# Performance work log

Hardware: AMD Instinct MI355X
Metric: run time of the kernel (lower is better)

## Reference

```python
import jax, jax.numpy as jnp
import numpy as np

# --- SLAYER params (nmnistNet.yaml) ---
THETA = 10.0
TS = 1.0
TAU_REF = 1.0
SCALE_REF = 2.0
T_SAMPLE = 300
B = 8

def _alpha_kernel(tau, mult, t_sample, ts, eps=0.01):
    vals = []
    t = 0.0
    while t < t_sample:
        v = mult * t / tau * np.exp(1.0 - t / tau)
        if abs(v) < eps and t > tau:
            break
        vals.append(v)
        t += ts
    return np.asarray(vals, np.float32)

# refractory kernel: alpha kernel with mult = -scaleRef*theta (slayer._calculateRefKernel)
REF_KERNEL = _alpha_kernel(TAU_REF, -SCALE_REF * THETA, T_SAMPLE, TS)
NREF = REF_KERNEL.shape[0]  # 11 for these params; REF_KERNEL[0] == 0


def spike(u):
    """slayerCuda.getSpikes: per-neuron sequential threshold recurrence over time.
    u: [..., T] membrane potential. On spike at t, REF_KERNEL is accumulated
    into u[t:t+NREF]; spike amplitude is 1/Ts."""
    uT = jnp.moveaxis(u, -1, 0)  # [T, ...]
    refk = jnp.asarray(REF_KERNEL[1:]).reshape((NREF - 1,) + (1,) * (u.ndim - 1))
    buf0 = jnp.zeros((NREF - 1,) + uT.shape[1:], u.dtype)  # pending refractory

    def step(buf, u_t):
        u_mod = u_t + buf[0]
        ev = (u_mod >= THETA).astype(u.dtype)
        buf = jnp.concatenate([buf[1:], jnp.zeros_like(buf[:1])], axis=0) + ev[None] * refk
        return buf, ev / TS

    _, s = jax.lax.scan(step, buf0, uT)
    return jnp.moveaxis(s, 0, -1)


def conv2d_t(x, w, pad):
    """slayer.conv: Conv3d with kernel (k,k,1) == per-timestep 2D conv.
    x: [B,C,H,W,T], w: [O,I,kh,kw]."""
    b, c, h, wd, t = x.shape
    xb = jnp.moveaxis(x, -1, 1).reshape(b * t, c, h, wd)
    y = jax.lax.conv_general_dilated(xb, w, (1, 1), [(pad, pad), (pad, pad)],
                                     dimension_numbers=('NCHW', 'OIHW', 'NCHW'))
    o, ho, wo = y.shape[1], y.shape[2], y.shape[3]
    return jnp.moveaxis(y.reshape(b, t, o, ho, wo), 1, -1)


def sum_pool2(x):
    """slayer.pool(2): fixed-weight (1.1*theta) 2x2/stride-2 sum over H,W per channel."""
    y = jax.lax.reduce_window(x, 0.0, jax.lax.add, (1, 1, 2, 2, 1), (1, 1, 2, 2, 1), 'VALID')
    return 1.1 * THETA * y


def setup_inputs():
    key = jax.random.key(0)
    k0, k1, k2, k3, k4 = jax.random.split(key, 5)
    spikeInput = (jax.random.uniform(k0, (B, 2, 34, 34, T_SAMPLE)) < 0.1).astype(jnp.float32) / TS
    # conv weights: kaiming-uniform bound * 100 (the __init__ scales conv weights by 100)
    w1 = jax.random.uniform(k1, (16, 2, 5, 5), minval=-14.1, maxval=14.1, dtype=jnp.float32)
    w2 = jax.random.uniform(k2, (32, 16, 3, 3), minval=-8.3, maxval=8.3, dtype=jnp.float32)
    w3 = jax.random.uniform(k3, (64, 32, 3, 3), minval=-5.9, maxval=5.9, dtype=jnp.float32)
    wfc = jax.random.uniform(k4, (10, 64, 8, 8), minval=-0.5, maxval=0.5, dtype=jnp.float32)
    return {"spikeInput": spikeInput, "w1": w1, "w2": w2, "w3": w3, "wfc": wfc}


def reference(spikeInput, w1, w2, w3, wfc):
    s1 = spike(conv2d_t(spikeInput, w1, 1))  # [B,16,32,32,T]
    s2 = spike(sum_pool2(s1))                # [B,16,16,16,T]
    s3 = spike(conv2d_t(s2, w2, 1))          # [B,32,16,16,T]
    s4 = spike(sum_pool2(s3))                # [B,32,8,8,T]
    s5 = spike(conv2d_t(s4, w3, 1))          # [B,64,8,8,T]
    # dense((8,8,64),10): Conv3d(64,10,(8,8,1)) == full-spatial contraction
    u = jnp.einsum('bchwt,ochw->bot', s5, wfc)[:, :, None, None, :]
    return spike(u)                          # [B,10,1,1,T]
```

## Files before the change

### kernel.cpp

```cpp
#include <hip/hip_runtime.h>
#include <hip/hip_bf16.h>
#include <cmath>

#define T_SAMPLE 300
#define NCHUNK 75

typedef __attribute__((ext_vector_type(8))) short short8;
typedef __attribute__((ext_vector_type(4))) float f32x4;

struct RefK { float v[10]; };

__device__ __forceinline__ unsigned char spike_step(float u, float* buf, const RefK& rk) {
    const float um = u + buf[0];
    const bool fire = um >= 10.0f;
    const float ev = fire ? 1.0f : 0.0f;
#pragma unroll
    for (int r = 0; r < 9; ++r) buf[r] = fmaf(ev, rk.v[r], buf[r + 1]);
    buf[9] = ev * rk.v[9];
    return fire ? (unsigned char)1 : (unsigned char)0;
}

__device__ __forceinline__ short8 bytes_to_bf16x8(uint2 w8) {
    union { uint4 u; short8 s8; } cv;
    cv.u.x = (w8.x & 0xFFu) * 0x3F80u | ((((w8.x >> 8) & 0xFFu) * 0x3F80u) << 16);
    cv.u.y = ((w8.x >> 16) & 0xFFu) * 0x3F80u | ((((w8.x >> 24) & 0xFFu) * 0x3F80u) << 16);
    cv.u.z = (w8.y & 0xFFu) * 0x3F80u | ((((w8.y >> 8) & 0xFFu) * 0x3F80u) << 16);
    cv.u.w = ((w8.y >> 16) & 0xFFu) * 0x3F80u | ((((w8.y >> 24) & 0xFFu) * 0x3F80u) << 16);
    return cv.s8;
}

__global__ __launch_bounds__(256) void transpose_in_k(
    const float* __restrict__ In, unsigned int* __restrict__ X)
{
    __shared__ unsigned int lds[16 * NCHUNK];
    const int blk = blockIdx.x;
    const int tn = threadIdx.x >> 4;
    const int tq = threadIdx.x & 15;
    const size_t n = (size_t)blk * 16 + tn;
#pragma unroll
    for (int p = 0; p < 5; ++p) {
        const int ch = p * 16 + tq;
        if (ch < NCHUNK) {
            const float4 v = *(const float4*)(In + n * T_SAMPLE + ch * 4);
            unsigned int u = (v.x != 0.f ? 1u : 0u) | (v.y != 0.f ? 0x100u : 0u) |
                             (v.z != 0.f ? 0x10000u : 0u) | (v.w != 0.f ? 0x1000000u : 0u);
            lds[tn * NCHUNK + ch] = u;
        }
    }
    __syncthreads();
    for (int idx = threadIdx.x; idx < 16 * NCHUNK; idx += 256) {
        const int ch = idx >> 4, t2 = idx & 15;
        X[(size_t)ch * 18496 + blk * 16 + t2] = lds[t2 * NCHUNK + ch];
    }
}

template <int IC, int OC, int K, int OH, int OW, int IH, int IW, int OPT, int CSPLIT>
__device__ __forceinline__ void conv_body(
    const uchar4* __restrict__ in_, const float* __restrict__ W,
    float4* __restrict__ U, int b0, int nbl)
{
    constexpr int TH = 8, TW = 8;
    constexpr int EH = TH + K - 1, EW = TW + K - 1;
    constexpr int EWP = EW + 1;
    constexpr int NTX = OW / TW, NTY = OH / TH, NT = NTX * NTY;
    constexpr int KK = K * K;
    constexpr int ICH = IC / CSPLIT;
    constexpr int ES = ICH * EH * EW;
    constexpr int PLANE_IN = 8 * IC * IH * IW;
    const int PLANE_U = nbl * OC * OH * OW;

    __shared__ float4 tile[ICH * EH * EWP];

    const int tc = blockIdx.x;
    const int by = blockIdx.y;
    const int til = by % NT;
    const int og = by / NT;
    const int ty = til / NTX, tx = til % NTX;
    const int bl = blockIdx.z;
    const int b = b0 + bl;
    const int tid = threadIdx.x;
    const int wave = tid >> 6, lane = tid & 63;
    const int py = lane >> 3, px = lane & 7;

    const int iy0 = ty * TH - 1, ix0 = tx * TW - 1;
    const uchar4* ib = in_ + (size_t)tc * PLANE_IN + (size_t)b * IC * IH * IW;

    float acc[OPT][4];
#pragma unroll
    for (int j = 0; j < OPT; ++j)
#pragma unroll
        for (int k = 0; k < 4; ++k) acc[j][k] = 0.f;

    int ob = (og * 4 + wave) * OPT;
    ob = __builtin_amdgcn_readfirstlane(ob);
    const float* Wp = W + (size_t)ob * IC * KK;

    for (int s = 0; s < CSPLIT; ++s) {
        if (s > 0) __syncthreads();
        for (int e = tid; e < ES; e += 256) {
            const int cl = e / (EH * EW);
            const int r = e % (EH * EW);
            const int iy = r / EW, ix = r % EW;
            const int gy = iy0 + iy, gx = ix0 + ix;
            float4 v = make_float4(0.f, 0.f, 0.f, 0.f);
            if ((unsigned)gy < (unsigned)IH && (unsigned)gx < (unsigned)IW) {
                const uchar4 sv = ib[((s * ICH + cl) * IH + gy) * IW + gx];
                v = make_float4((float)sv.x, (float)sv.y, (float)sv.z, (float)sv.w);
            }
            tile[(cl * EH + iy) * EWP + ix] = v;
        }
        __syncthreads();

        for (int cl = 0; cl < ICH; ++cl) {
            const int c = s * ICH + cl;
#pragma unroll
            for (int dy = 0; dy < K; ++dy) {
                float wr[OPT][K];
#pragma unroll
                for (int j = 0; j < OPT; ++j)
#pragma unroll
                    for (int dx = 0; dx < K; ++dx)
                        wr[j][dx] = Wp[(j * IC + c) * KK + dy * K + dx];
#pragma unroll
                for (int dx = 0; dx < K; ++dx) {
                    const float4 v = tile[((cl * EH) + py + dy) * EWP + (px + dx)];
#pragma unroll
                    for (int j = 0; j < OPT; ++j) {
                        const float w = wr[j][dx];
                        acc[j][0] = fmaf(w, v.x, acc[j][0]);
                        acc[j][1] = fmaf(w, v.y, acc[j][1]);
                        acc[j][2] = fmaf(w, v.z, acc[j][2]);
                        acc[j][3] = fmaf(w, v.w, acc[j][3]);
                    }
                }
            }
        }
    }

    const int y = ty * TH + py, x = tx * TW + px;
#pragma unroll
    for (int j = 0; j < OPT; ++j) {
        const int nb = ((bl * OC + (ob + j)) * OH + y) * OW + x;
        U[(size_t)tc * PLANE_U + nb] = make_float4(acc[j][0], acc[j][1], acc[j][2], acc[j][3]);
    }
}

__global__ __launch_bounds__(256) void conv1_k(
    const uchar4* __restrict__ in_, const float* __restrict__ W,
    float4* __restrict__ U, int b0, int nbl)
{ conv_body<2, 16, 5, 32, 32, 34, 34, 4, 1>(in_, W, U, b0, nbl); }

__global__ __launch_bounds__(256) void prep_w3_k(
    const float* __restrict__ w3, unsigned short* __restrict__ Wr)
{
    const int g = blockIdx.x * 256 + threadIdx.x;
    const int j = g & 7;
    const int lane = (g >> 3) & 63;
    const int mt = (g >> 9) & 3;
    const int rest = g >> 11;
    const int ks = rest % 9;
    const int s = rest / 9;
    const int oc = mt * 16 + (lane & 15);
    const int ic = (lane >> 4) * 8 + j;
    const float w = w3[(oc * 32 + ic) * 9 + ks];
    __hip_bfloat16 hb = __float2bfloat16(w);
    const float hf = __bfloat162float(hb);
    __hip_bfloat16 mb = __float2bfloat16(w - hf);
    const float mf = __bfloat162float(mb);
    __hip_bfloat16 lb = __float2bfloat16(w - hf - mf);
    __hip_bfloat16 sel = (s == 0) ? hb : ((s == 1) ? mb : lb);
    Wr[g] = *(unsigned short*)&sel;
}

__global__ __launch_bounds__(256) void prep_w2_k(
    const float* __restrict__ w2, unsigned short* __restrict__ Wr2)
{
    const int g = blockIdx.x * 256 + threadIdx.x;
    const int j = g & 7;
    const int lane = (g >> 3) & 63;
    const int mt = (g >> 9) & 1;
    const int rest = g >> 10;
    const int kp = rest % 5;
    const int s = rest / 5;
    const int q = lane >> 4;
    const int oc = mt * 16 + (lane & 15);
    const int tap = kp * 2 + (q >> 1);
    const int ic = (q & 1) * 8 + j;
    const float w = (tap <= 8) ? w2[(oc * 16 + ic) * 9 + tap] : 0.f;
    __hip_bfloat16 hb = __float2bfloat16(w);
    const float hf = __bfloat162float(hb);
    __hip_bfloat16 mb = __float2bfloat16(w - hf);
    const float mf = __bfloat162float(mb);
    __hip_bfloat16 lb = __float2bfloat16(w - hf - mf);
    __hip_bfloat16 sel = (s == 0) ? hb : ((s == 1) ? mb : lb);
    Wr2[g] = *(unsigned short*)&sel;
}

__global__ __launch_bounds__(256) void conv2_mfma_k(
    const unsigned int* __restrict__ s2u, const unsigned short* __restrict__ Wr2,
    float4* __restrict__ U, int b0, int nbl)
{
    __shared__ __align__(16) unsigned char pad[4 * 18 * 18 * 16];
    const int tc = blockIdx.x;
    const int bl = blockIdx.z;
    const int b = b0 + bl;
    const int tid = threadIdx.x;
    const int wv = tid >> 6, lane = tid & 63;
    const int q = lane >> 4, n = lane & 15;
    const int PLANE_U = nbl * 8192;

    unsigned int* lp = (unsigned int*)pad;
    for (int i = tid; i < 5184; i += 256) lp[i] = 0u;
    __syncthreads();
    const unsigned int* sb = s2u + (size_t)tc * 32768 + b * 4096;
    for (int e = tid; e < 4096; e += 256) {
        const unsigned int v = sb[e];
        const int c = e >> 8, pix = e & 255;
        const int base = (((pix >> 4) + 1) * 18 + ((pix & 15) + 1)) * 16 + c;
        pad[base]         = (unsigned char)(v & 0xFFu);
        pad[5184 + base]  = (unsigned char)((v >> 8) & 0xFFu);
        pad[10368 + base] = (unsigned char)((v >> 16) & 0xFFu);
        pad[15552 + base] = (unsigned char)(v >> 24);
    }
    __syncthreads();

    for (int i = 0; i < 4; ++i) {
        const int r = wv * 4 + i;
        f32x4 acc[2][4];
#pragma unroll
        for (int mt = 0; mt < 2; ++mt)
#pragma unroll
            for (int t = 0; t < 4; ++t) acc[mt][t] = (f32x4){0.f, 0.f, 0.f, 0.f};

        for (int kp = 0; kp < 5; ++kp) {
            short8 Af[6];
#pragma unroll
            for (int s = 0; s < 3; ++s)
#pragma unroll
                for (int mt = 0; mt < 2; ++mt)
                    Af[s * 2 + mt] = *(const short8*)(Wr2 + ((((s * 5 + kp) * 2 + mt) * 64 + lane) * 8));
            int tap = kp * 2 + (q >> 1);
            if (tap > 8) tap = 8;
            const int dy = tap / 3, dx = tap % 3;
#pragma unroll
            for (int t = 0; t < 4; ++t) {
                const int off = ((t * 18 + r + dy) * 18 + (n + dx)) * 16 + (q & 1) * 8;
                const short8 Bf = bytes_to_bf16x8(*(const uint2*)(pad + off));
#pragma unroll
                for (int s = 0; s < 3; ++s)
#pragma unroll
                    for (int mt = 0; mt < 2; ++mt)
                        acc[mt][t] = __builtin_amdgcn_mfma_f32_16x16x32_bf16(
                            Af[s * 2 + mt], Bf, acc[mt][t], 0, 0, 0);
            }
        }

        const size_t ub = (size_t)tc * PLANE_U;
#pragma unroll
        for (int mt = 0; mt < 2; ++mt)
#pragma unroll
            for (int rr = 0; rr < 4; ++rr) {
                const int oc = mt * 16 + q * 4 + rr;
                const int nb = (bl * 32 + oc) * 256 + r * 16 + n;
                U[ub + nb] = make_float4(acc[mt][0][rr], acc[mt][1][rr], acc[mt][2][rr], acc[mt][3][rr]);
            }
    }
}

__global__ __launch_bounds__(256) void conv3_mfma_k(
    const unsigned int* __restrict__ s4u, const unsigned short* __restrict__ Wr,
    float4* __restrict__ U)
{
    __shared__ __align__(16) unsigned char pad[12800];
    const int tc = blockIdx.x;
    const int bl = blockIdx.z;
    const int tid = threadIdx.x;
    const int wv = tid >> 6, lane = tid & 63;
    const int q = lane >> 4, n = lane & 15;

    unsigned int* lp = (unsigned int*)pad;
    for (int i = tid; i < 3200; i += 256) lp[i] = 0u;
    __syncthreads();
    const unsigned int* sb = s4u + (size_t)tc * 16384 + bl * 2048;
    for (int e = tid; e < 2048; e += 256) {
        const unsigned int v = sb[e];
        const int c = e >> 6, pix = e & 63;
        const int base = (((pix >> 3) + 1) * 10 + ((pix & 7) + 1)) * 32 + c;
        pad[base]        = (unsigned char)(v & 0xFFu);
        pad[3200 + base] = (unsigned char)((v >> 8) & 0xFFu);
        pad[6400 + base] = (unsigned char)((v >> 16) & 0xFFu);
        pad[9600 + base] = (unsigned char)(v >> 24);
    }
    __syncthreads();

    const int pixel = wv * 16 + n;
    const int py0 = pixel >> 3, px0 = pixel & 7;

    f32x4 acc[4][4];
#pragma unroll
    for (int mt = 0; mt < 4; ++mt)
#pragma unroll
        for (int t = 0; t < 4; ++t) acc[mt][t] = (f32x4){0.f, 0.f, 0.f, 0.f};

    for (int ks = 0; ks < 9; ++ks) {
        const int dy = ks / 3, dx = ks % 3;
        short8 Af[12];
#pragma unroll
        for (int s = 0; s < 3; ++s)
#pragma unroll
            for (int mt = 0; mt < 4; ++mt)
                Af[s * 4 + mt] = *(const short8*)(Wr + ((((s * 9 + ks) * 4 + mt) * 64 + lane) * 8));
#pragma unroll
        for (int t = 0; t < 4; ++t) {
            const int off = ((t * 10 + py0 + dy) * 10 + (px0 + dx)) * 32 + q * 8;
            const short8 Bf = bytes_to_bf16x8(*(const uint2*)(pad + off));
#pragma unroll
            for (int s = 0; s < 3; ++s)
#pragma unroll
                for (int mt = 0; mt < 4; ++mt)
                    acc[mt][t] = __builtin_amdgcn_mfma_f32_16x16x32_bf16(
                        Af[s * 4 + mt], Bf, acc[mt][t], 0, 0, 0);
        }
    }

    const size_t ub = (size_t)tc * 32768 + (size_t)bl * 4096;
#pragma unroll
    for (int mt = 0; mt < 4; ++mt)
#pragma unroll
        for (int r = 0; r < 4; ++r) {
            const int oc = mt * 16 + q * 4 + r;
            const int nb = oc * 64 + wv * 16 + n;
            U[ub + nb] = make_float4(acc[mt][0][r], acc[mt][1][r], acc[mt][2][r], acc[mt][3][r]);
        }
}

__device__ __forceinline__ void spike_body(
    const float4* __restrict__ U, uchar4* __restrict__ S,
    int nneur, int sstride, int soff, const RefK& rk)
{
    const int n = blockIdx.x * 64 + threadIdx.x;
    const float4* up = U + n;
    uchar4* sp = S + soff + n;
    float buf[10];
#pragma unroll
    for (int r = 0; r < 10; ++r) buf[r] = 0.f;

    float4 ring[8];
#pragma unroll
    for (int r = 0; r < 8; ++r) ring[r] = up[(size_t)r * nneur];

#pragma unroll 8
    for (int ch = 0; ch < 72; ++ch) {
        const float4 cur = ring[ch & 7];
        const int pf = (ch + 8 < NCHUNK) ? ch + 8 : NCHUNK - 1;
        ring[ch & 7] = up[(size_t)pf * nneur];
        uchar4 o;
        o.x = spike_step(cur.x, buf, rk);
        o.y = spike_step(cur.y, buf, rk);
        o.z = spike_step(cur.z, buf, rk);
        o.w = spike_step(cur.w, buf, rk);
        sp[(size_t)ch * sstride] = o;
    }
#pragma unroll
    for (int ch = 72; ch < NCHUNK; ++ch) {
        const float4 cur = ring[ch & 7];
        uchar4 o;
        o.x = spike_step(cur.x, buf, rk);
        o.y = spike_step(cur.y, buf, rk);
        o.z = spike_step(cur.z, buf, rk);
        o.w = spike_step(cur.w, buf, rk);
        sp[(size_t)ch * sstride] = o;
    }
}

__global__ __launch_bounds__(64) void spike1_k(
    const float4* U, uchar4* S, int nneur, int sstride, int soff, RefK rk)
{ spike_body(U, S, nneur, sstride, soff, rk); }

__global__ __launch_bounds__(64) void spike2_k(
    const float4* U, uchar4* S, int nneur, int sstride, int soff, RefK rk)
{ spike_body(U, S, nneur, sstride, soff, rk); }

__global__ __launch_bounds__(64) void spike3_k(
    const float4* U, uchar4* S, int nneur, int sstride, int soff, RefK rk)
{ spike_body(U, S, nneur, sstride, soff, rk); }

__device__ __forceinline__ int bsum4(uint2 r0, uint2 r1, int k) {
    return (int)((r0.x >> (8 * k)) & 0xffu) + (int)((r0.y >> (8 * k)) & 0xffu)
         + (int)((r1.x >> (8 * k)) & 0xffu) + (int)((r1.y >> (8 * k)) & 0xffu);
}

template <int C, int H, int W>
__device__ __forceinline__ void pool_body(
    const uchar4* __restrict__ Sin, uchar4* __restrict__ Sout, const RefK& rk)
{
    constexpr int H2 = H / 2, W2 = W / 2;
    constexpr int SIN = 8 * C * H * W;
    constexpr int SOUT = 8 * C * H2 * W2;
    const int n = blockIdx.x * 64 + threadIdx.x;
    const int x = n % W2;
    const int y = (n / W2) % H2;
    const int c = (n / (W2 * H2)) % C;
    const int b = n / (W2 * H2 * C);
    const int base = (((b * C + c) * H + 2 * y) * W + 2 * x);
    uchar4* q = Sout + n;

    float buf[10];
#pragma unroll
    for (int r = 0; r < 10; ++r) buf[r] = 0.f;

    uint2 r0[8], r1[8];
#pragma unroll
    for (int r = 0; r < 8; ++r) {
        r0[r] = *(const uint2*)(Sin + (size_t)r * SIN + base);
        r1[r] = *(const uint2*)(Sin + (size_t)r * SIN + base + W);
    }

#pragma unroll 8
    for (int ch = 0; ch < 72; ++ch) {
        const uint2 a0 = r0[ch & 7], a1 = r1[ch & 7];
        const int pf = (ch + 8 < NCHUNK) ? ch + 8 : NCHUNK - 1;
        r0[ch & 7] = *(const uint2*)(Sin + (size_t)pf * SIN + base);
        r1[ch & 7] = *(const uint2*)(Sin + (size_t)pf * SIN + base + W);
        uchar4 o;
        o.x = spike_step(11.0f * (float)bsum4(a0, a1, 0), buf, rk);
        o.y = spike_step(11.0f * (float)bsum4(a0, a1, 1), buf, rk);
        o.z = spike_step(11.0f * (float)bsum4(a0, a1, 2), buf, rk);
        o.w = spike_step(11.0f * (float)bsum4(a0, a1, 3), buf, rk);
        q[(size_t)ch * SOUT] = o;
    }
#pragma unroll
    for (int ch = 72; ch < NCHUNK; ++ch) {
        const uint2 a0 = r0[ch & 7], a1 = r1[ch & 7];
        uchar4 o;
        o.x = spike_step(11.0f * (float)bsum4(a0, a1, 0), buf, rk);
        o.y = spike_step(11.0f * (float)bsum4(a0, a1, 1), buf, rk);
        o.z = spike_step(11.0f * (float)bsum4(a0, a1, 2), buf, rk);
        o.w = spike_step(11.0f * (float)bsum4(a0, a1, 3), buf, rk);
        q[(size_t)ch * SOUT] = o;
    }
}

__global__ __launch_bounds__(64) void pool2_k(
    const uchar4* Sin, uchar4* Sout, RefK rk) { pool_body<16, 32, 32>(Sin, Sout, rk); }
__global__ __launch_bounds__(64) void pool4_k(
    const uchar4* Sin, uchar4* Sout, RefK rk) { pool_body<32, 16, 16>(Sin, Sout, rk); }

__global__ __launch_bounds__(64) void dense_k(
    const uchar4* __restrict__ S5, const float* __restrict__ WFC,
    float4* __restrict__ U6)
{
    const int tc = blockIdx.x, o = blockIdx.y, b = blockIdx.z;
    const int lane = threadIdx.x;
    float a0 = 0.f, a1 = 0.f, a2 = 0.f, a3 = 0.f;
    const uchar4* sb = S5 + (size_t)tc * 32768 + b * 4096;
    const float* wb = WFC + o * 4096;
    for (int i = 0; i < 64; ++i) {
        const int site = i * 64 + lane;
        const uchar4 s = sb[site];
        const float w = wb[site];
        a0 = fmaf(w, (float)s.x, a0);
        a1 = fmaf(w, (float)s.y, a1);
        a2 = fmaf(w, (float)s.z, a2);
        a3 = fmaf(w, (float)s.w, a3);
    }
#pragma unroll
    for (int m = 1; m < 64; m <<= 1) {
        a0 += __shfl_xor(a0, m, 64);
        a1 += __shfl_xor(a1, m, 64);
        a2 += __shfl_xor(a2, m, 64);
        a3 += __shfl_xor(a3, m, 64);
    }
    if (lane == 0)
        U6[(size_t)tc * 80 + b * 10 + o] = make_float4(a0, a1, a2, a3);
}

__global__ __launch_bounds__(128) void spike6_k(
    const float4* __restrict__ U6, float* __restrict__ Out, RefK rk)
{
    const int n = threadIdx.x;
    if (n >= 80) return;
    const float4* up = U6 + n;
    float* op = Out + (size_t)n * T_SAMPLE;
    float buf[10];
#pragma unroll
    for (int r = 0; r < 10; ++r) buf[r] = 0.f;

    float4 ring[8];
#pragma unroll
    for (int r = 0; r < 8; ++r) ring[r] = up[(size_t)r * 80];

#pragma unroll 8
    for (int ch = 0; ch < 72; ++ch) {
        const float4 cur = ring[ch & 7];
        const int pf = (ch + 8 < NCHUNK) ? ch + 8 : NCHUNK - 1;
        ring[ch & 7] = up[(size_t)pf * 80];
        float4 o;
        o.x = (float)spike_step(cur.x, buf, rk);
        o.y = (float)spike_step(cur.y, buf, rk);
        o.z = (float)spike_step(cur.z, buf, rk);
        o.w = (float)spike_step(cur.w, buf, rk);
        *(float4*)(op + ch * 4) = o;
    }
#pragma unroll
    for (int ch = 72; ch < NCHUNK; ++ch) {
        const float4 cur = ring[ch & 7];
        float4 o;
        o.x = (float)spike_step(cur.x, buf, rk);
        o.y = (float)spike_step(cur.y, buf, rk);
        o.z = (float)spike_step(cur.z, buf, rk);
        o.w = (float)spike_step(cur.w, buf, rk);
        *(float4*)(op + ch * 4) = o;
    }
}

extern "C" void kernel_launch(void* const* d_in, const int* in_sizes, int n_in,
                              void* d_out, int out_size, void* d_ws, size_t ws_size,
                              hipStream_t stream)
{
    const float* spikeIn = (const float*)d_in[0];
    const float* w1 = (const float*)d_in[1];
    const float* w2 = (const float*)d_in[2];
    const float* w3 = (const float*)d_in[3];
    const float* wfc = (const float*)d_in[4];
    float* out = (float*)d_out;

    RefK rk;
    for (int t = 1; t <= 10; ++t)
        rk.v[t - 1] = (float)(-20.0 * (double)t * std::exp(1.0 - (double)t));

    const size_t A_BYTES = 39321600;
    const size_t B_BYTES = 9830400;
    const size_t U6_BYTES = 96000;
    const size_t U_HUGE = 157286400, U_BIG = 78643200, U_SMALL = 39321600;
    const size_t TAIL = A_BYTES + B_BYTES + U6_BYTES;
    const bool huge = ws_size >= U_HUGE + TAIL;
    const bool big = ws_size >= U_BIG + TAIL;
    const size_t U_BYTES = huge ? U_HUGE : (big ? U_BIG : U_SMALL);

    char* ws = (char*)d_ws;
    float4* U = (float4*)ws;
    uchar4* A = (uchar4*)(ws + U_BYTES);
    uchar4* Bb = (uchar4*)(ws + U_BYTES + A_BYTES);
    float4* U6 = (float4*)(ws + U_BYTES + A_BYTES + B_BYTES);
    unsigned short* Wr = (unsigned short*)(ws + U_BYTES + 20971520);
    unsigned short* Wr2 = (unsigned short*)(ws + U_BYTES + 20971520 + 131072);

    uchar4* X = Bb;
    uchar4* s1 = A;
    uchar4* s2 = Bb;
    uchar4* s3 = A;
    uchar4* s4 = Bb;
    uchar4* s5 = A;

    transpose_in_k<<<18496 / 16, 256, 0, stream>>>(spikeIn, (unsigned int*)X);

    const int nbl1 = huge ? 8 : (big ? 4 : 2);
    for (int b0 = 0; b0 < 8; b0 += nbl1) {
        dim3 g1(NCHUNK, 16, nbl1);
        conv1_k<<<g1, 256, 0, stream>>>(X, w1, U, b0, nbl1);
        const int nn = nbl1 * 16384;
        spike1_k<<<nn / 64, 64, 0, stream>>>(U, s1, nn, 131072, b0 * 16384, rk);
    }
    pool2_k<<<32768 / 64, 64, 0, stream>>>(s1, s2, rk);
    prep_w2_k<<<60, 256, 0, stream>>>(w2, Wr2);
    prep_w3_k<<<216, 256, 0, stream>>>(w3, Wr);
    const int nbl2 = (huge || big) ? 8 : 4;
    for (int b0 = 0; b0 < 8; b0 += nbl2) {
        dim3 g2(NCHUNK, 1, nbl2);
        conv2_mfma_k<<<g2, 256, 0, stream>>>((const unsigned int*)s2, Wr2, U, b0, nbl2);
        const int nn = nbl2 * 8192;
        spike2_k<<<nn / 64, 64, 0, stream>>>(U, s3, nn, 65536, b0 * 8192, rk);
    }
    pool4_k<<<16384 / 64, 64, 0, stream>>>(s3, s4, rk);
    {
        dim3 g3(NCHUNK, 1, 8);
        conv3_mfma_k<<<g3, 256, 0, stream>>>((const unsigned int*)s4, Wr, U);
        spike3_k<<<32768 / 64, 64, 0, stream>>>(U, s5, 32768, 32768, 0, rk);
    }
    dim3 g6(NCHUNK, 10, 8);
    dense_k<<<g6, 64, 0, stream>>>(s5, wfc, U6);
    spike6_k<<<1, 128, 0, stream>>>(U6, out, rk);
}
```

Before: 300.9 us.

## Port conv1 to bf16 MFMA with split-weight precision and packed spike tiles

Replaces the scalar FP32 conv1 kernel with an MFMA-based version. The weights are pre-split into three bf16 parts (hi/mid/lo) so the FP32 result is kept nearly exact. The binary spike inputs are packed into LDS as bytes and expanded to bf16 fragments, and the 5x5x2 taps are laid out into a 6-wide slot K dimension. This is meant to cut conv1's FP32 FMA cost by using matrix cores. In exchange it adds a weight-prep kernel, does three MFMA passes per tap group, and carries some zero-padded slots.

```diff
diff --git a/kernel.cpp b/kernel.cpp
--- a/kernel.cpp
+++ b/kernel.cpp
@@ -29,6 +29,16 @@
     return cv.s8;
 }
 
+__device__ __forceinline__ unsigned short bf16_split_sel(float w, int s) {
+    __hip_bfloat16 hb = __float2bfloat16(w);
+    const float hf = __bfloat162float(hb);
+    __hip_bfloat16 mb = __float2bfloat16(w - hf);
+    const float mf = __bfloat162float(mb);
+    __hip_bfloat16 lb = __float2bfloat16(w - hf - mf);
+    __hip_bfloat16 sel = (s == 0) ? hb : ((s == 1) ? mb : lb);
+    return *(unsigned short*)&sel;
+}
+
 __global__ __launch_bounds__(256) void transpose_in_k(
     const float* __restrict__ In, unsigned int* __restrict__ X)
 {
@@ -54,101 +64,22 @@
     }
 }
 
-template <int IC, int OC, int K, int OH, int OW, int IH, int IW, int OPT, int CSPLIT>
-__device__ __forceinline__ void conv_body(
-    const uchar4* __restrict__ in_, const float* __restrict__ W,
-    float4* __restrict__ U, int b0, int nbl)
-{
-    constexpr int TH = 8, TW = 8;
-    constexpr int EH = TH + K - 1, EW = TW + K - 1;
-    constexpr int EWP = EW + 1;
-    constexpr int NTX = OW / TW, NTY = OH / TH, NT = NTX * NTY;
-    constexpr int KK = K * K;
-    constexpr int ICH = IC / CSPLIT;
-    constexpr int ES = ICH * EH * EW;
-    constexpr int PLANE_IN = 8 * IC * IH * IW;
-    const int PLANE_U = nbl * OC * OH * OW;
-
-    __shared__ float4 tile[ICH * EH * EWP];
-
-    const int tc = blockIdx.x;
-    const int by = blockIdx.y;
-    const int til = by % NT;
-    const int og = by / NT;
-    const int ty = til / NTX, tx = til % NTX;
-    const int bl = blockIdx.z;
-    const int b = b0 + bl;
-    const int tid = threadIdx.x;
-    const int wave = tid >> 6, lane = tid & 63;
-    const int py = lane >> 3, px = lane & 7;
-
-    const int iy0 = ty * TH - 1, ix0 = tx * TW - 1;
-    const uchar4* ib = in_ + (size_t)tc * PLANE_IN + (size_t)b * IC * IH * IW;
-
-    float acc[OPT][4];
-#pragma unroll
-    for (int j = 0; j < OPT; ++j)
-#pragma unroll
-        for (int k = 0; k < 4; ++k) acc[j][k] = 0.f;
-
-    int ob = (og * 4 + wave) * OPT;
-    ob = __builtin_amdgcn_readfirstlane(ob);
-    const float* Wp = W + (size_t)ob * IC * KK;
-
-    for (int s = 0; s < CSPLIT; ++s) {
-        if (s > 0) __syncthreads();
-        for (int e = tid; e < ES; e += 256) {
-            const int cl = e / (EH * EW);
-            const int r = e % (EH * EW);
-            const int iy = r / EW, ix = r % EW;
-            const int gy = iy0 + iy, gx = ix0 + ix;
-            float4 v = make_float4(0.f, 0.f, 0.f, 0.f);
-            if ((unsigned)gy < (unsigned)IH && (unsigned)gx < (unsigned)IW) {
-                const uchar4 sv = ib[((s * ICH + cl) * IH + gy) * IW + gx];
-                v = make_float4((float)sv.x, (float)sv.y, (float)sv.z, (float)sv.w);
-            }
-            tile[(cl * EH + iy) * EWP + ix] = v;
-        }
-        __syncthreads();
-
-        for (int cl = 0; cl < ICH; ++cl) {
-            const int c = s * ICH + cl;
-#pragma unroll
-            for (int dy = 0; dy < K; ++dy) {
-                float wr[OPT][K];
-#pragma unroll
-                for (int j = 0; j < OPT; ++j)
-#pragma unroll
-                    for (int dx = 0; dx < K; ++dx)
-                        wr[j][dx] = Wp[(j * IC + c) * KK + dy * K + dx];
-#pragma unroll
-                for (int dx = 0; dx < K; ++dx) {
-                    const float4 v = tile[((cl * EH) + py + dy) * EWP + (px + dx)];
-#pragma unroll
-                    for (int j = 0; j < OPT; ++j) {
-                        const float w = wr[j][dx];
-                        acc[j][0] = fmaf(w, v.x, acc[j][0]);
-                        acc[j][1] = fmaf(w, v.y, acc[j][1]);
-                        acc[j][2] = fmaf(w, v.z, acc[j][2]);
-                        acc[j][3] = fmaf(w, v.w, acc[j][3]);
-                    }
-                }
-            }
-        }
-    }
-
-    const int y = ty * TH + py, x = tx * TW + px;
-#pragma unroll
-    for (int j = 0; j < OPT; ++j) {
-        const int nb = ((bl * OC + (ob + j)) * OH + y) * OW + x;
-        U[(size_t)tc * PLANE_U + nb] = make_float4(acc[j][0], acc[j][1], acc[j][2], acc[j][3]);
-    }
-}
-
-__global__ __launch_bounds__(256) void conv1_k(
-    const uchar4* __restrict__ in_, const float* __restrict__ W,
-    float4* __restrict__ U, int b0, int nbl)
-{ conv_body<2, 16, 5, 32, 32, 34, 34, 4, 1>(in_, W, U, b0, nbl); }
+__global__ __launch_bounds__(256) void prep_w1_k(
+    const float* __restrict__ w1, unsigned short* __restrict__ Wr1)
+{
+    const int g = blockIdx.x * 256 + threadIdx.x;
+    const int j = g & 7;
+    const int lane = (g >> 3) & 63;
+    const int ks = (g >> 9) & 3;
+    const int s = g >> 11;
+    const int q = lane >> 4;
+    const int oc = lane & 15;
+    const int kg = ks * 32 + q * 8 + j;
+    const int slot = kg >> 2, c = kg & 1;
+    const int dy = slot / 6, dx = slot % 6;
+    const float w = (dy < 5 && dx < 5) ? w1[((oc * 2 + c) * 5 + dy) * 5 + dx] * 0.5f : 0.f;
+    Wr1[g] = bf16_split_sel(w, s);
+}
 
 __global__ __launch_bounds__(256) void prep_w3_k(
     const float* __restrict__ w3, unsigned short* __restrict__ Wr)
@@ -162,14 +93,7 @@
     const int s = rest / 9;
     const int oc = mt * 16 + (lane & 15);
     const int ic = (lane >> 4) * 8 + j;
-    const float w = w3[(oc * 32 + ic) * 9 + ks];
-    __hip_bfloat16 hb = __float2bfloat16(w);
-    const float hf = __bfloat162float(hb);
-    __hip_bfloat16 mb = __float2bfloat16(w - hf);
-    const float mf = __bfloat162float(mb);
-    __hip_bfloat16 lb = __float2bfloat16(w - hf - mf);
-    __hip_bfloat16 sel = (s == 0) ? hb : ((s == 1) ? mb : lb);
-    Wr[g] = *(unsigned short*)&sel;
+    Wr[g] = bf16_split_sel(w3[(oc * 32 + ic) * 9 + ks], s);
 }
 
 __global__ __launch_bounds__(256) void prep_w2_k(
@@ -187,13 +111,86 @@
     const int tap = kp * 2 + (q >> 1);
     const int ic = (q & 1) * 8 + j;
     const float w = (tap <= 8) ? w2[(oc * 16 + ic) * 9 + tap] : 0.f;
-    __hip_bfloat16 hb = __float2bfloat16(w);
-    const float hf = __bfloat162float(hb);
-    __hip_bfloat16 mb = __float2bfloat16(w - hf);
-    const float mf = __bfloat162float(mb);
-    __hip_bfloat16 lb = __float2bfloat16(w - hf - mf);
-    __hip_bfloat16 sel = (s == 0) ? hb : ((s == 1) ? mb : lb);
-    Wr2[g] = *(unsigned short*)&sel;
+    Wr2[g] = bf16_split_sel(w, s);
+}
+
+__global__ __launch_bounds__(256) void conv1_mfma_k(
+    const unsigned int* __restrict__ Xu, const unsigned short* __restrict__ Wr1,
+    float4* __restrict__ U, int b0, int nbl)
+{
+    __shared__ __align__(16) unsigned int pad[768];
+    const int tc = blockIdx.x;
+    const int tile = blockIdx.y;
+    const int ty = tile >> 2, tx = tile & 3;
+    const int bl = blockIdx.z;
+    const int b = b0 + bl;
+    const int tid = threadIdx.x;
+    const int wv = tid >> 6, lane = tid & 63;
+    const int q = lane >> 4, n = lane & 15;
+    const int PLANE_U = nbl * 16384;
+
+    for (int i = tid; i < 768; i += 256) pad[i] = 0u;
+    __syncthreads();
+    const unsigned int* xb = Xu + (size_t)tc * 18496;
+    if (tid < 192) {
+        const int r = tid >> 4, col = tid & 15;
+        const int y = ty * 8 + r - 1, x = tx * 8 + col - 1;
+        unsigned int w0 = 0u, w1v = 0u;
+        if ((unsigned)y < 34u && (unsigned)x < 34u) {
+            w0 = xb[((b * 2 + 0) * 34 + y) * 34 + x];
+            w1v = xb[((b * 2 + 1) * 34 + y) * 34 + x];
+        }
+#pragma unroll
+        for (int t = 0; t < 4; ++t) {
+            const unsigned int b0b = (w0 >> (8 * t)) & 0xFFu;
+            const unsigned int b1b = (w1v >> (8 * t)) & 0xFFu;
+            pad[(t * 12 + r) * 16 + col] = b0b | (b1b << 8) | (b0b << 16) | (b1b << 24);
+        }
+    }
+    __syncthreads();
+
+    const int pixel = wv * 16 + n;
+    const int py0 = pixel >> 3, px0 = pixel & 7;
+
+    short8 Af[12];
+#pragma unroll
+    for (int s = 0; s < 3; ++s)
+#pragma unroll
+        for (int ks = 0; ks < 4; ++ks)
+            Af[s * 4 + ks] = *(const short8*)(Wr1 + (((s * 4 + ks) * 64 + lane) * 8));
+
+    f32x4 acc[4];
+#pragma unroll
+    for (int t = 0; t < 4; ++t) acc[t] = (f32x4){0.f, 0.f, 0.f, 0.f};
+
+#pragma unroll
+    for (int ks = 0; ks < 4; ++ks) {
+        const int slotA = ks * 8 + q * 2, slotB = slotA + 1;
+        const int dyA = slotA / 6, dxA = slotA - dyA * 6;
+        const int dyB = slotB / 6, dxB = slotB - dyB * 6;
+        const int trA = min(py0 + dyA, 11), trB = min(py0 + dyB, 11);
+        const int tcA = px0 + dxA, tcB = px0 + dxB;
+#pragma unroll
+        for (int t = 0; t < 4; ++t) {
+            uint2 w8;
+            w8.x = pad[(t * 12 + trA) * 16 + tcA];
+            w8.y = pad[(t * 12 + trB) * 16 + tcB];
+            const short8 Bf = bytes_to_bf16x8(w8);
+#pragma unroll
+            for (int s = 0; s < 3; ++s)
+                acc[t] = __builtin_amdgcn_mfma_f32_16x16x32_bf16(
+                    Af[s * 4 + ks], Bf, acc[t], 0, 0, 0);
+        }
+    }
+
+    const int y = ty * 8 + py0, x = tx * 8 + px0;
+    const size_t ub = (size_t)tc * PLANE_U;
+#pragma unroll
+    for (int rr = 0; rr < 4; ++rr) {
+        const int oc = q * 4 + rr;
+        const int nb = (bl * 16 + oc) * 1024 + y * 32 + x;
+        U[ub + nb] = make_float4(acc[0][rr], acc[1][rr], acc[2][rr], acc[3][rr]);
+    }
 }
 
 __global__ __launch_bounds__(256) void conv2_mfma_k(
@@ -545,6 +542,7 @@
     float4* U6 = (float4*)(ws + U_BYTES + A_BYTES + B_BYTES);
     unsigned short* Wr = (unsigned short*)(ws + U_BYTES + 20971520);
     unsigned short* Wr2 = (unsigned short*)(ws + U_BYTES + 20971520 + 131072);
+    unsigned short* Wr1 = (unsigned short*)(ws + U_BYTES + A_BYTES + 5570560);
 
     uchar4* X = Bb;
     uchar4* s1 = A;
@@ -554,11 +552,12 @@
     uchar4* s5 = A;
 
     transpose_in_k<<<18496 / 16, 256, 0, stream>>>(spikeIn, (unsigned int*)X);
+    prep_w1_k<<<24, 256, 0, stream>>>(w1, Wr1);
 
     const int nbl1 = huge ? 8 : (big ? 4 : 2);
     for (int b0 = 0; b0 < 8; b0 += nbl1) {
         dim3 g1(NCHUNK, 16, nbl1);
-        conv1_k<<<g1, 256, 0, stream>>>(X, w1, U, b0, nbl1);
+        conv1_mfma_k<<<g1, 256, 0, stream>>>((const unsigned int*)X, Wr1, U, b0, nbl1);
         const int nn = nbl1 * 16384;
         spike1_k<<<nn / 64, 64, 0, stream>>>(U, s1, nn, 131072, b0 * 16384, rk);
     }
```

Measured after the change: 287.7 us. -4.4%, faster.
